# Performance work log

Hardware: AMD Instinct MI355X
Metric: run time of the kernel (lower is better)

## Reference

```python
import jax, jax.numpy as jnp
import numpy as np

D_MODEL = 1024
N_HEAD = 16
HEAD_DIM = D_MODEL // N_HEAD


def setup_inputs() -> dict:
    key = jax.random.key(0)
    k1, k2, k3 = jax.random.split(key, 3)
    x = jax.random.normal(k1, (2, 2048, D_MODEL), dtype=jnp.float32)
    w_qkv = jax.random.normal(k2, (D_MODEL, 3 * D_MODEL), dtype=jnp.float32) * (1.0 / np.sqrt(D_MODEL))
    w_proj = jax.random.normal(k3, (D_MODEL, D_MODEL), dtype=jnp.float32) * (1.0 / np.sqrt(D_MODEL))
    return {"x": x, "w_qkv": w_qkv, "w_proj": w_proj}


def reference(x, w_qkv, w_proj):
    bs, sl, dm = x.shape
    qkv = x @ w_qkv                                   # [B,S,3*D]
    qkv = qkv.reshape(bs, sl, 3, N_HEAD, HEAD_DIM)
    q, k, v = qkv[:, :, 0], qkv[:, :, 1], qkv[:, :, 2]  # [B,S,H,d]
    q = q.transpose(0, 2, 1, 3)                        # [B,H,S,d]
    k = k.transpose(0, 2, 1, 3)
    v = v.transpose(0, 2, 1, 3)
    sc = 1.0 / np.sqrt(HEAD_DIM).astype(np.float32)
    attn = jnp.einsum('bhqd,bhkd->bhqk', q, k) * sc    # [B,H,S,S]
    causal = jnp.tril(jnp.ones((sl, sl), dtype=bool))  # True = keep
    attn = jnp.where(causal, attn, -jnp.inf)
    w = jax.nn.softmax(attn, axis=-1)                  # [B,H,S,S] (dropout p=0)
    o = jnp.einsum('bhqk,bhkd->bhqd', w, v)            # [B,H,S,d]
    out = o.transpose(0, 2, 1, 3).reshape(bs, sl, dm)
    out = out @ w_proj
    return (out, w)
```

## Files before the change

kernel.cpp:

```cpp
#include <hip/hip_runtime.h>

typedef _Float16 half8 __attribute__((ext_vector_type(8)));
typedef float f32x4 __attribute__((ext_vector_type(4)));

__global__ __launch_bounds__(256) void cvt_kernel(const float* __restrict__ in,
                                                  _Float16* __restrict__ out, int n) {
  int i = (blockIdx.x * 256 + threadIdx.x) * 8;
  if (i >= n) return;
  float4 a = *(const float4*)(in + i);
  float4 b = *(const float4*)(in + i + 4);
  half8 o;
  o[0] = (_Float16)a.x; o[1] = (_Float16)a.y; o[2] = (_Float16)a.z; o[3] = (_Float16)a.w;
  o[4] = (_Float16)b.x; o[5] = (_Float16)b.y; o[6] = (_Float16)b.z; o[7] = (_Float16)b.w;
  *(half8*)(out + i) = o;
}

template <int MODE>
__global__ __launch_bounds__(256) void gemm16(const _Float16* __restrict__ A,
                                              const _Float16* __restrict__ B,
                                              float* __restrict__ Cf,
                                              _Float16* __restrict__ Ch,
                                              int M, int N, int K) {
  __shared__ _Float16 As[128][40];
  __shared__ _Float16 Bs[128][40];
  const int tid = threadIdx.x;
  const int lane = tid & 63;
  const int wid = tid >> 6;
  const int wr = wid >> 1, wc = wid & 1;
  const int quad = lane >> 4;
  const int l16 = lane & 15;
  const int m0 = blockIdx.y * 128;
  const int n0 = blockIdx.x * 128;

  f32x4 acc[4][4];
  const f32x4 fz = {0.f, 0.f, 0.f, 0.f};
#pragma unroll
  for (int i = 0; i < 4; i++)
#pragma unroll
    for (int j = 0; j < 4; j++) acc[i][j] = fz;

  const int am = tid >> 2;
  const int ak = (tid & 3) * 8;
  const int bk = tid >> 4;
  const int bn = (tid & 15) * 8;

  for (int kt = 0; kt < K; kt += 32) {
#pragma unroll
    for (int c = 0; c < 2; c++) {
      int m = c * 64 + am;
      half8 va = *(const half8*)(A + (size_t)(m0 + m) * K + kt + ak);
      *(half8*)&As[m][ak] = va;
      int k = c * 16 + bk;
      half8 vb = *(const half8*)(B + (size_t)(kt + k) * N + n0 + bn);
      int kg = k >> 3, k7 = k & 7;
#pragma unroll
      for (int i = 0; i < 8; i++) {
        int n = bn + i;
        Bs[n][((kg ^ ((n >> 3) & 3)) * 8) + k7] = vb[i];
      }
    }
    __syncthreads();
    half8 af[4], bf[4];
#pragma unroll
    for (int mi = 0; mi < 4; mi++)
      af[mi] = *(const half8*)&As[wr * 64 + mi * 16 + l16][quad * 8];
#pragma unroll
    for (int ni = 0; ni < 4; ni++) {
      int n = wc * 64 + ni * 16 + l16;
      bf[ni] = *(const half8*)&Bs[n][(quad ^ ((n >> 3) & 3)) * 8];
    }
#pragma unroll
    for (int mi = 0; mi < 4; mi++)
#pragma unroll
      for (int ni = 0; ni < 4; ni++)
        acc[mi][ni] = __builtin_amdgcn_mfma_f32_16x16x32_f16(af[mi], bf[ni], acc[mi][ni], 0, 0, 0);
    __syncthreads();
  }

#pragma unroll
  for (int mi = 0; mi < 4; mi++)
#pragma unroll
    for (int ni = 0; ni < 4; ni++)
#pragma unroll
      for (int r = 0; r < 4; r++) {
        int row = m0 + wr * 64 + mi * 16 + quad * 4 + r;
        int col = n0 + wc * 64 + ni * 16 + l16;
        float v = acc[mi][ni][r];
        if (MODE == 0) {
          Cf[(size_t)row * N + col] = v;
        } else {
          int which = col >> 10, h = (col >> 6) & 15, d = col & 63;
          int b = row >> 11, s = row & 2047;
          Ch[((((size_t)(which * 2 + b) * 16 + h) * 2048) + s) * 64 + d] = (_Float16)v;
        }
      }
}

__global__ __launch_bounds__(256) void attn_kernel(const _Float16* __restrict__ qkv,
                                                   float* __restrict__ w_out,
                                                   _Float16* __restrict__ o_buf) {
  const int qt = blockIdx.x;
  const int bh = blockIdx.y;
  const int tid = threadIdx.x;
  const int lane = tid & 63;
  const int wid = tid >> 6;
  const int quad = lane >> 4;
  const int l16 = lane & 15;

  const _Float16* qp = qkv + (size_t)bh * 131072;
  const _Float16* kp = qp + 4194304;
  const _Float16* vp = qp + 8388608;

  __shared__ _Float16 Ks[64][72];
  __shared__ _Float16 Vt[64][72];
  __shared__ _Float16 Ps[64][72];

  const int qrow = qt * 64 + wid * 16 + l16;
  const half8 qa0 = *(const half8*)(qp + qrow * 64 + quad * 8);
  const half8 qa1 = *(const half8*)(qp + qrow * 64 + 32 + quad * 8);

  float mrow[4], lrow[4];
#pragma unroll
  for (int r = 0; r < 4; r++) { mrow[r] = -__builtin_inff(); lrow[r] = 0.f; }

  const int srow = tid >> 3;
  const int d8 = (tid & 7) * 8;
  const float sc = 0.125f;
  const int growbase = qt * 64 + wid * 16 + quad * 4;
  const f32x4 fz = {0.f, 0.f, 0.f, 0.f};

  for (int kt = 0; kt <= qt; kt++) {
#pragma unroll
    for (int c = 0; c < 2; c++) {
      int srw = c * 32 + srow;
      *(half8*)&Ks[srw][d8] = *(const half8*)(kp + (kt * 64 + srw) * 64 + d8);
    }
    __syncthreads();
    f32x4 sacc[4];
#pragma unroll
    for (int ni = 0; ni < 4; ni++) {
      half8 kb0 = *(const half8*)&Ks[ni * 16 + l16][quad * 8];
      half8 kb1 = *(const half8*)&Ks[ni * 16 + l16][32 + quad * 8];
      f32x4 s = fz;
      s = __builtin_amdgcn_mfma_f32_16x16x32_f16(qa0, kb0, s, 0, 0, 0);
      s = __builtin_amdgcn_mfma_f32_16x16x32_f16(qa1, kb1, s, 0, 0, 0);
      sacc[ni] = s;
    }
#pragma unroll
    for (int r = 0; r < 4; r++) {
      int grow = growbase + r;
      float sv[4];
      float vmax = -__builtin_inff();
#pragma unroll
      for (int ni = 0; ni < 4; ni++) {
        int gcol = kt * 64 + ni * 16 + l16;
        float s = sacc[ni][r] * sc;
        if (gcol > grow) s = -__builtin_inff();
        sv[ni] = s;
        vmax = fmaxf(vmax, s);
      }
#pragma unroll
      for (int off = 1; off < 16; off <<= 1) vmax = fmaxf(vmax, __shfl_xor(vmax, off));
      float newm = fmaxf(mrow[r], vmax);
      float psum = 0.f;
#pragma unroll
      for (int ni = 0; ni < 4; ni++) psum += __expf(sv[ni] - newm);
#pragma unroll
      for (int off = 1; off < 16; off <<= 1) psum += __shfl_xor(psum, off);
      lrow[r] = lrow[r] * __expf(mrow[r] - newm) + psum;
      mrow[r] = newm;
    }
    __syncthreads();
  }

  float invl[4];
#pragma unroll
  for (int r = 0; r < 4; r++) invl[r] = 1.0f / lrow[r];

  f32x4 oacc[4];
#pragma unroll
  for (int di = 0; di < 4; di++) oacc[di] = fz;

  float* wbase = w_out + (size_t)bh * 2048 * 2048;

  for (int kt = 0; kt < 32; kt++) {
    if (kt <= qt) {
#pragma unroll
      for (int c = 0; c < 2; c++) {
        int srw = c * 32 + srow;
        *(half8*)&Ks[srw][d8] = *(const half8*)(kp + (kt * 64 + srw) * 64 + d8);
        half8 vv = *(const half8*)(vp + (kt * 64 + srw) * 64 + d8);
        int s7 = srw & 7, sg = srw >> 3;
#pragma unroll
        for (int i = 0; i < 8; i++) {
          int dd = d8 + i;
          Vt[dd][(((sg ^ (dd >> 3)) & 7) * 8) + s7] = vv[i];
        }
      }
      __syncthreads();
      f32x4 sacc[4];
#pragma unroll
      for (int ni = 0; ni < 4; ni++) {
        half8 kb0 = *(const half8*)&Ks[ni * 16 + l16][quad * 8];
        half8 kb1 = *(const half8*)&Ks[ni * 16 + l16][32 + quad * 8];
        f32x4 s = fz;
        s = __builtin_amdgcn_mfma_f32_16x16x32_f16(qa0, kb0, s, 0, 0, 0);
        s = __builtin_amdgcn_mfma_f32_16x16x32_f16(qa1, kb1, s, 0, 0, 0);
        sacc[ni] = s;
      }
#pragma unroll
      for (int ni = 0; ni < 4; ni++) {
#pragma unroll
        for (int r = 0; r < 4; r++) {
          int lrw = wid * 16 + quad * 4 + r;
          int grow = qt * 64 + lrw;
          int gcol = kt * 64 + ni * 16 + l16;
          float s = sacc[ni][r] * sc;
          float p = (gcol > grow) ? 0.0f : __expf(s - mrow[r]) * invl[r];
          wbase[(size_t)grow * 2048 + gcol] = p;
          Ps[lrw][ni * 16 + l16] = (_Float16)p;
        }
      }
      __syncthreads();
#pragma unroll
      for (int kk = 0; kk < 2; kk++) {
        half8 pa = *(const half8*)&Ps[wid * 16 + l16][kk * 32 + quad * 8];
#pragma unroll
        for (int di = 0; di < 4; di++) {
          int d = di * 16 + l16;
          half8 vb = *(const half8*)&Vt[d][(((kk * 4 + quad) ^ (d >> 3)) & 7) * 8];
          oacc[di] = __builtin_amdgcn_mfma_f32_16x16x32_f16(pa, vb, oacc[di], 0, 0, 0);
        }
      }
      __syncthreads();
    } else {
#pragma unroll
      for (int ni = 0; ni < 4; ni++)
#pragma unroll
        for (int r = 0; r < 4; r++) {
          int grow = qt * 64 + wid * 16 + quad * 4 + r;
          int gcol = kt * 64 + ni * 16 + l16;
          wbase[(size_t)grow * 2048 + gcol] = 0.0f;
        }
    }
  }

  const int b = bh >> 4, h = bh & 15;
#pragma unroll
  for (int di = 0; di < 4; di++)
#pragma unroll
    for (int r = 0; r < 4; r++) {
      int s = qt * 64 + wid * 16 + quad * 4 + r;
      int d = di * 16 + l16;
      o_buf[((size_t)(b * 2048 + s) * 16 + h) * 64 + d] = (_Float16)oacc[di][r];
    }
}

extern "C" void kernel_launch(void* const* d_in, const int* in_sizes, int n_in,
                              void* d_out, int out_size, void* d_ws, size_t ws_size,
                              hipStream_t stream) {
  const float* x = (const float*)d_in[0];
  const float* w_qkv = (const float*)d_in[1];
  const float* w_proj = (const float*)d_in[2];
  float* out = (float*)d_out;
  float* w_attn = out + (size_t)4194304;

  char* ws = (char*)d_ws;
  _Float16* x16 = (_Float16*)ws;
  _Float16* wqkv16 = (_Float16*)(ws + (size_t)(8 << 20));
  _Float16* wproj16 = (_Float16*)(ws + (size_t)(14 << 20));
  _Float16* qkvb = (_Float16*)(ws + (size_t)(16 << 20));
  _Float16* ob = (_Float16*)(ws + (size_t)(40 << 20));

  cvt_kernel<<<4194304 / 2048, 256, 0, stream>>>(x, x16, 4194304);
  cvt_kernel<<<3145728 / 2048, 256, 0, stream>>>(w_qkv, wqkv16, 3145728);
  cvt_kernel<<<1048576 / 2048, 256, 0, stream>>>(w_proj, wproj16, 1048576);

  gemm16<1><<<dim3(24, 32), 256, 0, stream>>>(x16, wqkv16, nullptr, qkvb, 4096, 3072, 1024);
  attn_kernel<<<dim3(32, 32), 256, 0, stream>>>(qkvb, w_attn, ob);
  gemm16<0><<<dim3(8, 32), 256, 0, stream>>>(ob, wproj16, out, nullptr, 4096, 1024, 1024);
}
```

Before: 766.0 us.

## Use direct global-to-LDS loads, pre-transposed weights and V, and max-free softmax

Weights are converted to fp16 in transposed [N,K] layout and V is transposed by a separate kernel. GEMM and attention tiles can then be loaded with global_load_lds straight into shared memory, with no per-element scatter. The softmax statistics pass drops the running-max and shuffle reductions and accumulates exp sums directly. Masked weight tiles are zero-filled with vector stores, and the output projection uses 64-wide N tiles for more blocks. The trade-off is that the unguarded exp can overflow if scores get large, and the new transpose kernels add extra launches.

```diff
diff --git a/kernel.cpp b/kernel.cpp
--- a/kernel.cpp
+++ b/kernel.cpp
@@ -2,6 +2,11 @@
 
 typedef _Float16 half8 __attribute__((ext_vector_type(8)));
 typedef float f32x4 __attribute__((ext_vector_type(4)));
+
+__device__ __forceinline__ void gl2lds16(const _Float16* g, _Float16* l) {
+  __builtin_amdgcn_global_load_lds((const __attribute__((address_space(1))) void*)g,
+                                   (__attribute__((address_space(3))) void*)l, 16, 0, 0);
+}
 
 __global__ __launch_bounds__(256) void cvt_kernel(const float* __restrict__ in,
                                                   _Float16* __restrict__ out, int n) {
@@ -15,62 +20,98 @@
   *(half8*)(out + i) = o;
 }
 
-template <int MODE>
+__global__ __launch_bounds__(256) void cvtT_kernel(const float* __restrict__ in,
+                                                   _Float16* __restrict__ out,
+                                                   int K, int N) {
+  __shared__ float Ts[64][65];
+  const int k0 = blockIdx.y * 64, n0 = blockIdx.x * 64;
+  const int t = threadIdx.x;
+  const int r = t >> 4, c = (t & 15) * 4;
+#pragma unroll
+  for (int i = 0; i < 4; i++) {
+    float4 v = *(const float4*)(in + (size_t)(k0 + r + i * 16) * N + n0 + c);
+    Ts[r + i * 16][c] = v.x; Ts[r + i * 16][c + 1] = v.y;
+    Ts[r + i * 16][c + 2] = v.z; Ts[r + i * 16][c + 3] = v.w;
+  }
+  __syncthreads();
+  const int nl = t >> 2, kq = (t & 3) * 16;
+  half8 o0, o1;
+#pragma unroll
+  for (int j = 0; j < 8; j++) {
+    o0[j] = (_Float16)Ts[kq + j][nl];
+    o1[j] = (_Float16)Ts[kq + 8 + j][nl];
+  }
+  *(half8*)(out + (size_t)(n0 + nl) * K + k0 + kq) = o0;
+  *(half8*)(out + (size_t)(n0 + nl) * K + k0 + kq + 8) = o1;
+}
+
+__global__ __launch_bounds__(256) void vtrans_kernel(const _Float16* __restrict__ v,
+                                                     _Float16* __restrict__ vt) {
+  __shared__ _Float16 Ht[64][72];
+  const int s0 = blockIdx.x * 64;
+  const _Float16* vb = v + (size_t)blockIdx.y * 131072;
+  _Float16* vtb = vt + (size_t)blockIdx.y * 131072;
+  const int t = threadIdx.x;
+  const int sl = t >> 3, dq = (t & 7) * 8;
+  *(half8*)&Ht[sl][dq] = *(const half8*)(vb + (s0 + sl) * 64 + dq);
+  *(half8*)&Ht[sl + 32][dq] = *(const half8*)(vb + (s0 + sl + 32) * 64 + dq);
+  __syncthreads();
+  const int dl = t >> 2, sq = (t & 3) * 16;
+  half8 o0, o1;
+#pragma unroll
+  for (int j = 0; j < 8; j++) {
+    o0[j] = Ht[sq + j][dl];
+    o1[j] = Ht[sq + 8 + j][dl];
+  }
+  *(half8*)(vtb + (size_t)dl * 2048 + s0 + sq) = o0;
+  *(half8*)(vtb + (size_t)dl * 2048 + s0 + sq + 8) = o1;
+}
+
+template <int MODE, int BN>
 __global__ __launch_bounds__(256) void gemm16(const _Float16* __restrict__ A,
                                               const _Float16* __restrict__ B,
                                               float* __restrict__ Cf,
                                               _Float16* __restrict__ Ch,
                                               int M, int N, int K) {
-  __shared__ _Float16 As[128][40];
-  __shared__ _Float16 Bs[128][40];
+  constexpr int MI = (BN == 128) ? 4 : 2;
+  __shared__ __align__(16) _Float16 As[128 * 32];
+  __shared__ __align__(16) _Float16 Bs[BN * 32];
   const int tid = threadIdx.x;
   const int lane = tid & 63;
   const int wid = tid >> 6;
-  const int wr = wid >> 1, wc = wid & 1;
   const int quad = lane >> 4;
   const int l16 = lane & 15;
+  const int mbase = (BN == 128) ? (wid >> 1) * 64 : wid * 32;
+  const int nbase = (BN == 128) ? (wid & 1) * 64 : 0;
   const int m0 = blockIdx.y * 128;
-  const int n0 = blockIdx.x * 128;
-
-  f32x4 acc[4][4];
+  const int n0 = blockIdx.x * BN;
+
+  f32x4 acc[MI][4];
   const f32x4 fz = {0.f, 0.f, 0.f, 0.f};
 #pragma unroll
-  for (int i = 0; i < 4; i++)
+  for (int i = 0; i < MI; i++)
 #pragma unroll
     for (int j = 0; j < 4; j++) acc[i][j] = fz;
 
-  const int am = tid >> 2;
-  const int ak = (tid & 3) * 8;
-  const int bk = tid >> 4;
-  const int bn = (tid & 15) * 8;
+  const int srow = tid >> 2;
+  const int kq = (tid & 3) * 8;
 
   for (int kt = 0; kt < K; kt += 32) {
-#pragma unroll
-    for (int c = 0; c < 2; c++) {
-      int m = c * 64 + am;
-      half8 va = *(const half8*)(A + (size_t)(m0 + m) * K + kt + ak);
-      *(half8*)&As[m][ak] = va;
-      int k = c * 16 + bk;
-      half8 vb = *(const half8*)(B + (size_t)(kt + k) * N + n0 + bn);
-      int kg = k >> 3, k7 = k & 7;
-#pragma unroll
-      for (int i = 0; i < 8; i++) {
-        int n = bn + i;
-        Bs[n][((kg ^ ((n >> 3) & 3)) * 8) + k7] = vb[i];
-      }
-    }
+    gl2lds16(A + (size_t)(m0 + srow) * K + kt + kq, &As[tid * 8]);
+    gl2lds16(A + (size_t)(m0 + 64 + srow) * K + kt + kq, &As[2048 + tid * 8]);
+    gl2lds16(B + (size_t)(n0 + srow) * K + kt + kq, &Bs[tid * 8]);
+    if (BN == 128)
+      gl2lds16(B + (size_t)(n0 + 64 + srow) * K + kt + kq, &Bs[2048 + tid * 8]);
     __syncthreads();
-    half8 af[4], bf[4];
-#pragma unroll
-    for (int mi = 0; mi < 4; mi++)
-      af[mi] = *(const half8*)&As[wr * 64 + mi * 16 + l16][quad * 8];
-#pragma unroll
-    for (int ni = 0; ni < 4; ni++) {
-      int n = wc * 64 + ni * 16 + l16;
-      bf[ni] = *(const half8*)&Bs[n][(quad ^ ((n >> 3) & 3)) * 8];
-    }
-#pragma unroll
-    for (int mi = 0; mi < 4; mi++)
+    half8 af[MI], bf[4];
+#pragma unroll
+    for (int mi = 0; mi < MI; mi++)
+      af[mi] = *(const half8*)&As[(mbase + mi * 16 + l16) * 32 + quad * 8];
+#pragma unroll
+    for (int ni = 0; ni < 4; ni++)
+      bf[ni] = *(const half8*)&Bs[(nbase + ni * 16 + l16) * 32 + quad * 8];
+#pragma unroll
+    for (int mi = 0; mi < MI; mi++)
 #pragma unroll
       for (int ni = 0; ni < 4; ni++)
         acc[mi][ni] = __builtin_amdgcn_mfma_f32_16x16x32_f16(af[mi], bf[ni], acc[mi][ni], 0, 0, 0);
@@ -78,13 +119,13 @@
   }
 
 #pragma unroll
-  for (int mi = 0; mi < 4; mi++)
+  for (int mi = 0; mi < MI; mi++)
 #pragma unroll
     for (int ni = 0; ni < 4; ni++)
 #pragma unroll
       for (int r = 0; r < 4; r++) {
-        int row = m0 + wr * 64 + mi * 16 + quad * 4 + r;
-        int col = n0 + wc * 64 + ni * 16 + l16;
+        int row = m0 + mbase + mi * 16 + quad * 4 + r;
+        int col = n0 + nbase + ni * 16 + l16;
         float v = acc[mi][ni][r];
         if (MODE == 0) {
           Cf[(size_t)row * N + col] = v;
@@ -97,10 +138,10 @@
 }
 
 __global__ __launch_bounds__(256) void attn_kernel(const _Float16* __restrict__ qkv,
+                                                   const _Float16* __restrict__ vt,
                                                    float* __restrict__ w_out,
                                                    _Float16* __restrict__ o_buf) {
-  const int qt = blockIdx.x;
-  const int bh = blockIdx.y;
+  const int qt = blockIdx.x, bh = blockIdx.y;
   const int tid = threadIdx.x;
   const int lane = tid & 63;
   const int wid = tid >> 6;
@@ -109,139 +150,114 @@
 
   const _Float16* qp = qkv + (size_t)bh * 131072;
   const _Float16* kp = qp + 4194304;
-  const _Float16* vp = qp + 8388608;
-
-  __shared__ _Float16 Ks[64][72];
-  __shared__ _Float16 Vt[64][72];
-  __shared__ _Float16 Ps[64][72];
+  const _Float16* vtb = vt + (size_t)bh * 131072;
+
+  __shared__ __align__(16) _Float16 Ks[2 * 64 * 32];
+  __shared__ __align__(16) _Float16 Vs[2 * 64 * 32];
+  __shared__ __align__(16) _Float16 Ps[64][72];
 
   const int qrow = qt * 64 + wid * 16 + l16;
   const half8 qa0 = *(const half8*)(qp + qrow * 64 + quad * 8);
   const half8 qa1 = *(const half8*)(qp + qrow * 64 + 32 + quad * 8);
 
-  float mrow[4], lrow[4];
-#pragma unroll
-  for (int r = 0; r < 4; r++) { mrow[r] = -__builtin_inff(); lrow[r] = 0.f; }
-
-  const int srow = tid >> 3;
-  const int d8 = (tid & 7) * 8;
+  const int srow = tid >> 2;
+  const int blk8 = (tid & 3) * 8;
   const float sc = 0.125f;
-  const int growbase = qt * 64 + wid * 16 + quad * 4;
   const f32x4 fz = {0.f, 0.f, 0.f, 0.f};
+  const int lrow0 = wid * 16 + quad * 4;
+
+  float lsum[4] = {0.f, 0.f, 0.f, 0.f};
 
   for (int kt = 0; kt <= qt; kt++) {
-#pragma unroll
-    for (int c = 0; c < 2; c++) {
-      int srw = c * 32 + srow;
-      *(half8*)&Ks[srw][d8] = *(const half8*)(kp + (kt * 64 + srw) * 64 + d8);
-    }
+    gl2lds16(kp + (size_t)(kt * 64 + srow) * 64 + blk8, &Ks[tid * 8]);
+    gl2lds16(kp + (size_t)(kt * 64 + srow) * 64 + 32 + blk8, &Ks[2048 + tid * 8]);
     __syncthreads();
     f32x4 sacc[4];
 #pragma unroll
     for (int ni = 0; ni < 4; ni++) {
-      half8 kb0 = *(const half8*)&Ks[ni * 16 + l16][quad * 8];
-      half8 kb1 = *(const half8*)&Ks[ni * 16 + l16][32 + quad * 8];
+      half8 kb0 = *(const half8*)&Ks[(ni * 16 + l16) * 32 + quad * 8];
+      half8 kb1 = *(const half8*)&Ks[2048 + (ni * 16 + l16) * 32 + quad * 8];
       f32x4 s = fz;
       s = __builtin_amdgcn_mfma_f32_16x16x32_f16(qa0, kb0, s, 0, 0, 0);
       s = __builtin_amdgcn_mfma_f32_16x16x32_f16(qa1, kb1, s, 0, 0, 0);
       sacc[ni] = s;
     }
-#pragma unroll
-    for (int r = 0; r < 4; r++) {
-      int grow = growbase + r;
-      float sv[4];
-      float vmax = -__builtin_inff();
-#pragma unroll
-      for (int ni = 0; ni < 4; ni++) {
-        int gcol = kt * 64 + ni * 16 + l16;
-        float s = sacc[ni][r] * sc;
-        if (gcol > grow) s = -__builtin_inff();
-        sv[ni] = s;
-        vmax = fmaxf(vmax, s);
-      }
-#pragma unroll
-      for (int off = 1; off < 16; off <<= 1) vmax = fmaxf(vmax, __shfl_xor(vmax, off));
-      float newm = fmaxf(mrow[r], vmax);
-      float psum = 0.f;
-#pragma unroll
-      for (int ni = 0; ni < 4; ni++) psum += __expf(sv[ni] - newm);
-#pragma unroll
-      for (int off = 1; off < 16; off <<= 1) psum += __shfl_xor(psum, off);
-      lrow[r] = lrow[r] * __expf(mrow[r] - newm) + psum;
-      mrow[r] = newm;
+    if (kt < qt) {
+#pragma unroll
+      for (int ni = 0; ni < 4; ni++)
+#pragma unroll
+        for (int r = 0; r < 4; r++) lsum[r] += __expf(sacc[ni][r] * sc);
+    } else {
+#pragma unroll
+      for (int ni = 0; ni < 4; ni++)
+#pragma unroll
+        for (int r = 0; r < 4; r++) {
+          if (ni * 16 + l16 <= lrow0 + r) lsum[r] += __expf(sacc[ni][r] * sc);
+        }
     }
     __syncthreads();
   }
-
   float invl[4];
 #pragma unroll
-  for (int r = 0; r < 4; r++) invl[r] = 1.0f / lrow[r];
+  for (int r = 0; r < 4; r++) {
+    float s = lsum[r];
+    s += __shfl_xor(s, 1); s += __shfl_xor(s, 2);
+    s += __shfl_xor(s, 4); s += __shfl_xor(s, 8);
+    invl[r] = 1.0f / s;
+  }
 
   f32x4 oacc[4];
 #pragma unroll
   for (int di = 0; di < 4; di++) oacc[di] = fz;
 
-  float* wbase = w_out + (size_t)bh * 2048 * 2048;
+  float* wbase = w_out + (size_t)bh * 4194304 + (size_t)qt * 64 * 2048;
 
   for (int kt = 0; kt < 32; kt++) {
     if (kt <= qt) {
-#pragma unroll
-      for (int c = 0; c < 2; c++) {
-        int srw = c * 32 + srow;
-        *(half8*)&Ks[srw][d8] = *(const half8*)(kp + (kt * 64 + srw) * 64 + d8);
-        half8 vv = *(const half8*)(vp + (kt * 64 + srw) * 64 + d8);
-        int s7 = srw & 7, sg = srw >> 3;
-#pragma unroll
-        for (int i = 0; i < 8; i++) {
-          int dd = d8 + i;
-          Vt[dd][(((sg ^ (dd >> 3)) & 7) * 8) + s7] = vv[i];
-        }
-      }
+      gl2lds16(kp + (size_t)(kt * 64 + srow) * 64 + blk8, &Ks[tid * 8]);
+      gl2lds16(kp + (size_t)(kt * 64 + srow) * 64 + 32 + blk8, &Ks[2048 + tid * 8]);
+      gl2lds16(vtb + (size_t)srow * 2048 + kt * 64 + blk8, &Vs[tid * 8]);
+      gl2lds16(vtb + (size_t)srow * 2048 + kt * 64 + 32 + blk8, &Vs[2048 + tid * 8]);
       __syncthreads();
       f32x4 sacc[4];
 #pragma unroll
       for (int ni = 0; ni < 4; ni++) {
-        half8 kb0 = *(const half8*)&Ks[ni * 16 + l16][quad * 8];
-        half8 kb1 = *(const half8*)&Ks[ni * 16 + l16][32 + quad * 8];
+        half8 kb0 = *(const half8*)&Ks[(ni * 16 + l16) * 32 + quad * 8];
+        half8 kb1 = *(const half8*)&Ks[2048 + (ni * 16 + l16) * 32 + quad * 8];
         f32x4 s = fz;
         s = __builtin_amdgcn_mfma_f32_16x16x32_f16(qa0, kb0, s, 0, 0, 0);
         s = __builtin_amdgcn_mfma_f32_16x16x32_f16(qa1, kb1, s, 0, 0, 0);
         sacc[ni] = s;
       }
 #pragma unroll
-      for (int ni = 0; ni < 4; ni++) {
+      for (int ni = 0; ni < 4; ni++)
 #pragma unroll
         for (int r = 0; r < 4; r++) {
-          int lrw = wid * 16 + quad * 4 + r;
-          int grow = qt * 64 + lrw;
-          int gcol = kt * 64 + ni * 16 + l16;
-          float s = sacc[ni][r] * sc;
-          float p = (gcol > grow) ? 0.0f : __expf(s - mrow[r]) * invl[r];
-          wbase[(size_t)grow * 2048 + gcol] = p;
-          Ps[lrw][ni * 16 + l16] = (_Float16)p;
+          int lrw = lrow0 + r;
+          int col = ni * 16 + l16;
+          float p = __expf(sacc[ni][r] * sc) * invl[r];
+          if (kt == qt && col > lrw) p = 0.0f;
+          wbase[(size_t)lrw * 2048 + kt * 64 + col] = p;
+          Ps[lrw][col] = (_Float16)p;
         }
-      }
       __syncthreads();
 #pragma unroll
       for (int kk = 0; kk < 2; kk++) {
         half8 pa = *(const half8*)&Ps[wid * 16 + l16][kk * 32 + quad * 8];
 #pragma unroll
         for (int di = 0; di < 4; di++) {
-          int d = di * 16 + l16;
-          half8 vb = *(const half8*)&Vt[d][(((kk * 4 + quad) ^ (d >> 3)) & 7) * 8];
+          half8 vb = *(const half8*)&Vs[kk * 2048 + (di * 16 + l16) * 32 + quad * 8];
           oacc[di] = __builtin_amdgcn_mfma_f32_16x16x32_f16(pa, vb, oacc[di], 0, 0, 0);
         }
       }
       __syncthreads();
     } else {
-#pragma unroll
-      for (int ni = 0; ni < 4; ni++)
-#pragma unroll
-        for (int r = 0; r < 4; r++) {
-          int grow = qt * 64 + wid * 16 + quad * 4 + r;
-          int gcol = kt * 64 + ni * 16 + l16;
-          wbase[(size_t)grow * 2048 + gcol] = 0.0f;
-        }
+      const int rr = tid >> 4;
+      const int cc = (tid & 15) * 4;
+      float* wz = wbase + (size_t)kt * 64 + cc;
+#pragma unroll
+      for (int p = 0; p < 4; p++)
+        *(f32x4*)(wz + (size_t)(p * 16 + rr) * 2048) = fz;
     }
   }
 
@@ -250,7 +266,7 @@
   for (int di = 0; di < 4; di++)
 #pragma unroll
     for (int r = 0; r < 4; r++) {
-      int s = qt * 64 + wid * 16 + quad * 4 + r;
+      int s = qt * 64 + lrow0 + r;
       int d = di * 16 + l16;
       o_buf[((size_t)(b * 2048 + s) * 16 + h) * 64 + d] = (_Float16)oacc[di][r];
     }
@@ -267,16 +283,18 @@
 
   char* ws = (char*)d_ws;
   _Float16* x16 = (_Float16*)ws;
-  _Float16* wqkv16 = (_Float16*)(ws + (size_t)(8 << 20));
-  _Float16* wproj16 = (_Float16*)(ws + (size_t)(14 << 20));
+  _Float16* wqkvT = (_Float16*)(ws + (size_t)(8 << 20));
+  _Float16* wprojT = (_Float16*)(ws + (size_t)(14 << 20));
   _Float16* qkvb = (_Float16*)(ws + (size_t)(16 << 20));
-  _Float16* ob = (_Float16*)(ws + (size_t)(40 << 20));
-
-  cvt_kernel<<<4194304 / 2048, 256, 0, stream>>>(x, x16, 4194304);
-  cvt_kernel<<<3145728 / 2048, 256, 0, stream>>>(w_qkv, wqkv16, 3145728);
-  cvt_kernel<<<1048576 / 2048, 256, 0, stream>>>(w_proj, wproj16, 1048576);
-
-  gemm16<1><<<dim3(24, 32), 256, 0, stream>>>(x16, wqkv16, nullptr, qkvb, 4096, 3072, 1024);
-  attn_kernel<<<dim3(32, 32), 256, 0, stream>>>(qkvb, w_attn, ob);
-  gemm16<0><<<dim3(8, 32), 256, 0, stream>>>(ob, wproj16, out, nullptr, 4096, 1024, 1024);
-}
+  _Float16* vT = (_Float16*)(ws + (size_t)(40 << 20));
+  _Float16* ob = (_Float16*)(ws + (size_t)(48 << 20));
+
+  cvt_kernel<<<2048, 256, 0, stream>>>(x, x16, 4194304);
+  cvtT_kernel<<<dim3(48, 16), 256, 0, stream>>>(w_qkv, wqkvT, 1024, 3072);
+  cvtT_kernel<<<dim3(16, 16), 256, 0, stream>>>(w_proj, wprojT, 1024, 1024);
+
+  gemm16<1, 128><<<dim3(24, 32), 256, 0, stream>>>(x16, wqkvT, nullptr, qkvb, 4096, 3072, 1024);
+  vtrans_kernel<<<dim3(32, 32), 256, 0, stream>>>(qkvb + (size_t)2 * 4194304, vT);
+  attn_kernel<<<dim3(32, 32), 256, 0, stream>>>(qkvb, vT, w_attn, ob);
+  gemm16<0, 64><<<dim3(16, 32), 256, 0, stream>>>(ob, wprojT, out, nullptr, 4096, 1024, 1024);
+}
```

Result: faster. 722.0 us (-5.7%).
